# Optimization experiments

Measured on AMD Instinct MI355X. Metric: run time of the kernel, lower is better.

## Reference

```python
import jax, jax.numpy as jnp
import numpy as np

B, S, HID = 2, 4096, 768
H, DH = 12, 64
FF = 3072
W = 128  # one-sided attention band; window span = 2*W+1
EPS = 1e-12


def _ln(x, g, b):
    m = jnp.mean(x, axis=-1, keepdims=True)
    v = jnp.var(x, axis=-1, keepdims=True)
    return (x - m) * jax.lax.rsqrt(v + EPS) * g + b


def _band_attend(q, k, v, dmask, w):
    # q,k,v: (B,H,S,D) fp32; dmask: (B,S,2w+1) additive key-mask. Returns (B,S,H,D).
    b, h, s, d = q.shape
    nc = s // w
    qc = q.reshape(b, h, nc, w, d)
    pad = ((0, 0), (0, 0), (w, w), (0, 0))
    kp = jnp.pad(k, pad)
    vp = jnp.pad(v, pad)
    win = jnp.arange(nc)[:, None] * w + jnp.arange(3 * w)[None, :]  # (nc, 3w) indices into padded seq
    kc = kp[:, :, win]  # (B,H,nc,3w,D)
    vc = vp[:, :, win]
    s3 = jnp.einsum('bhcxd,bhcyd->bhcxy', qc, kc)  # (B,H,nc,w,3w)
    # extract band: query i in chunk attends keys j in [i, i+2w] of the 3w window
    off = jnp.arange(w)[:, None] + jnp.arange(2 * w + 1)[None, :]  # (w, 2w+1)
    band = jnp.take_along_axis(s3, off[None, None, None], axis=-1)  # (B,H,nc,w,2w+1)
    band = band.reshape(b, h, s, 2 * w + 1)
    keypos = jnp.arange(s)[:, None] + jnp.arange(-w, w + 1)[None, :]
    valid = (keypos >= 0) & (keypos < s)  # mask_invalid_locations
    band = jnp.where(valid[None, None], band, -1e30)
    band = band + dmask[:, None]
    p = jax.nn.softmax(band, axis=-1)
    # scatter probs back to chunk-dense (w, 3w) layout for the PV matmul
    pc = p.reshape(b, h, nc, w, 2 * w + 1)
    j = jnp.arange(3 * w)[None, :] - jnp.arange(w)[:, None]  # (w,3w) offset indices
    ok = (j >= 0) & (j <= 2 * w)
    jcl = jnp.clip(j, 0, 2 * w)
    pdense = jnp.take_along_axis(pc, jcl[None, None, None], axis=-1)  # (B,H,nc,w,3w)
    pdense = jnp.where(ok[None, None, None], pdense, 0.0)
    ctx = jnp.einsum('bhcxy,bhcyd->bhcxd', pdense, vc)  # (B,H,nc,w,D)
    return ctx.reshape(b, h, s, d).transpose(0, 2, 1, 3)


def setup_inputs() -> dict:
    key = jax.random.key(0)
    ks = jax.random.split(key, 8)
    sc = 0.02
    inp = {
        'hidden_states': jax.random.normal(ks[0], (B, S, HID), jnp.float32),
        'attention_mask': jax.random.randint(ks[1], (B, 1, 1, S), 0, 2, jnp.int32),
        'Wq': jax.random.normal(ks[2], (HID, HID), jnp.float32) * sc,
        'bq': jnp.zeros((HID,), jnp.float32),
        'Wk': jax.random.normal(ks[3], (HID, HID), jnp.float32) * sc,
        'bk': jnp.zeros((HID,), jnp.float32),
        'Wv': jax.random.normal(ks[4], (HID, HID), jnp.float32) * sc,
        'bv': jnp.zeros((HID,), jnp.float32),
        'Wd': jax.random.normal(ks[5], (HID, HID), jnp.float32) * sc,
        'bd': jnp.zeros((HID,), jnp.float32),
        'ln1_g': jnp.ones((HID,), jnp.float32),
        'ln1_b': jnp.zeros((HID,), jnp.float32),
        'Wf': jax.random.normal(ks[6], (HID, FF), jnp.float32) * sc,
        'bf': jnp.zeros((FF,), jnp.float32),
        'Wo': jax.random.normal(ks[7], (FF, HID), jnp.float32) * sc,
        'bo': jnp.zeros((HID,), jnp.float32),
        'ln2_g': jnp.ones((HID,), jnp.float32),
        'ln2_b': jnp.zeros((HID,), jnp.float32),
    }
    return inp


def reference(hidden_states, attention_mask, Wq, bq, Wk, bk, Wv, bv, Wd, bd,
              ln1_g, ln1_b, Wf, bf, Wo, bo, ln2_g, ln2_b):
    def heads(x):
        return x.reshape(B, S, H, DH).transpose(0, 2, 1, 3)  # (B,H,S,DH)

    q = heads(hidden_states @ Wq + bq).astype(jnp.float32) / np.float32(np.sqrt(DH))
    k = heads(hidden_states @ Wk + bk).astype(jnp.float32)
    v = heads(hidden_states @ Wv + bv).astype(jnp.float32)

    am = attention_mask.reshape(B, S)
    maskvals = jnp.where(am != 0, -10000.0, 0.0).astype(jnp.float32)  # (B,S)
    mpad = jnp.pad(maskvals, ((0, 0), (W, W)))
    kidx = jnp.arange(S)[:, None] + jnp.arange(2 * W + 1)[None, :]
    dmask = mpad[:, kidx]  # (B,S,2w+1)

    ctx = _band_attend(q, k, v, dmask, W)  # (B,S,H,DH)

    w_d = Wd.reshape(H, DH, HID)
    proj = jnp.einsum('bfnd,ndh->bfh', ctx, w_d) + bd
    attn_out = _ln(hidden_states + proj, ln1_g, ln1_b)

    ff = jax.nn.gelu(attn_out @ Wf + bf, approximate=False)
    ff = ff @ Wo + bo
    return _ln(ff + attn_out, ln2_g, ln2_b)
```

## Files before the change

### kernel.cpp

```cpp
#include <hip/hip_runtime.h>
#include <cstdint>
#include <cstddef>

#define S_LEN 4096
#define HIDD 768
#define NH 12
#define FFD 3072

typedef float f32x4 __attribute__((ext_vector_type(4)));
typedef short s16x8 __attribute__((ext_vector_type(8)));
typedef short s16x4 __attribute__((ext_vector_type(4)));

__device__ __forceinline__ short f2bf(float f) {
  unsigned u = __float_as_uint(f);
  u += 0x7fffu + ((u >> 16) & 1u);
  return (short)(u >> 16);
}
__device__ __forceinline__ float bf2f(short s) {
  return __uint_as_float(((unsigned)(unsigned short)s) << 16);
}

__global__ void convx_k(const float* __restrict__ x, short* __restrict__ o) {
  size_t i = (size_t)blockIdx.x * 256 + threadIdx.x;
  float4 f = ((const float4*)x)[i];
  s16x4 v;
  v[0] = f2bf(f.x); v[1] = f2bf(f.y); v[2] = f2bf(f.z); v[3] = f2bf(f.w);
  ((s16x4*)o)[i] = v;
}

__global__ void wtrans_k(const float* __restrict__ Wq, const float* __restrict__ Wk,
                         const float* __restrict__ Wv, const float* __restrict__ Wd,
                         const float* __restrict__ Wf, const float* __restrict__ Wo,
                         short* __restrict__ oq, short* __restrict__ ok_,
                         short* __restrict__ ov, short* __restrict__ od,
                         short* __restrict__ of_, short* __restrict__ oo) {
  __shared__ float tl[64][65];
  int id = blockIdx.x;
  const float* in; short* out; int R, C, tr, tc;
  if (id < 576) {
    int wsel = id / 144; int t = id % 144; tr = t / 12; tc = t % 12; R = 768; C = 768;
    in = wsel == 0 ? Wq : wsel == 1 ? Wk : wsel == 2 ? Wv : Wd;
    out = wsel == 0 ? oq : wsel == 1 ? ok_ : wsel == 2 ? ov : od;
  } else if (id < 1152) {
    int t = id - 576; tr = t / 48; tc = t % 48; R = 768; C = 3072; in = Wf; out = of_;
  } else {
    int t = id - 1152; tr = t / 12; tc = t % 12; R = 3072; C = 768; in = Wo; out = oo;
  }
  int r0 = tr * 64, c0 = tc * 64;
  int tid = threadIdx.x;
  #pragma unroll
  for (int i = 0; i < 16; i++) {
    int idx = i * 256 + tid; int r = idx >> 6, cc = idx & 63;
    tl[r][cc] = in[(size_t)(r0 + r) * C + c0 + cc];
  }
  __syncthreads();
  #pragma unroll
  for (int i = 0; i < 16; i++) {
    int idx = i * 256 + tid; int cc = idx >> 6, rr = idx & 63;
    out[(size_t)(c0 + cc) * R + r0 + rr] = f2bf(tl[rr][cc]);
  }
}

__global__ void vtrans_k(const short* __restrict__ vh, short* __restrict__ vth) {
  __shared__ short tl[64][72];
  int s0 = blockIdx.x * 64; int bh = blockIdx.y;
  int tid = threadIdx.x;
  const short* base = vh + ((size_t)bh << 18);
  #pragma unroll
  for (int i = 0; i < 16; i++) {
    int idx = i * 256 + tid; int r = idx >> 6, cc = idx & 63;
    tl[r][cc] = base[(size_t)(s0 + r) * 64 + cc];
  }
  __syncthreads();
  short* ob = vth + ((size_t)bh << 18);
  #pragma unroll
  for (int i = 0; i < 16; i++) {
    int idx = i * 256 + tid; int dh = idx >> 6, s = idx & 63;
    ob[((size_t)dh << 12) + s0 + s] = tl[s][dh];
  }
}

template <int EPI>
__global__ void __launch_bounds__(256) gemm_bt(
    const short* __restrict__ A, const short* __restrict__ Bt,
    const float* __restrict__ bias, const void* __restrict__ resid,
    void* __restrict__ out, int N, int K, float scale) {
  __shared__ short As[128 * 72];
  __shared__ short Bs[128 * 72];
  const int tid = threadIdx.x;
  const int lane = tid & 63;
  const int w = tid >> 6;
  const int wr = w >> 1, wc = w & 1;
  const int m0 = blockIdx.x * 128, n0 = blockIdx.y * 128;
  f32x4 acc[4][4];
  #pragma unroll
  for (int i = 0; i < 4; i++)
    #pragma unroll
    for (int j = 0; j < 4; j++) { acc[i][j][0] = 0.f; acc[i][j][1] = 0.f; acc[i][j][2] = 0.f; acc[i][j][3] = 0.f; }

  for (int k0 = 0; k0 < K; k0 += 64) {
    #pragma unroll
    for (int i = 0; i < 4; i++) {
      int ch = tid + i * 256;
      int row = ch >> 3, seg = ch & 7;
      *(s16x8*)&As[row * 72 + seg * 8] = *(const s16x8*)&A[(size_t)(m0 + row) * K + k0 + seg * 8];
      *(s16x8*)&Bs[row * 72 + seg * 8] = *(const s16x8*)&Bt[(size_t)(n0 + row) * K + k0 + seg * 8];
    }
    __syncthreads();
    const int kc = (lane >> 4) * 8;
    #pragma unroll
    for (int ks = 0; ks < 2; ks++) {
      s16x8 af[4], bfr[4];
      #pragma unroll
      for (int mt = 0; mt < 4; mt++)
        af[mt] = *(const s16x8*)&As[(wr * 64 + mt * 16 + (lane & 15)) * 72 + ks * 32 + kc];
      #pragma unroll
      for (int nt = 0; nt < 4; nt++)
        bfr[nt] = *(const s16x8*)&Bs[(wc * 64 + nt * 16 + (lane & 15)) * 72 + ks * 32 + kc];
      #pragma unroll
      for (int mt = 0; mt < 4; mt++)
        #pragma unroll
        for (int nt = 0; nt < 4; nt++)
          acc[mt][nt] = __builtin_amdgcn_mfma_f32_16x16x32_bf16(af[mt], bfr[nt], acc[mt][nt], 0, 0, 0);
    }
    __syncthreads();
  }
  #pragma unroll
  for (int nt = 0; nt < 4; nt++) {
    const int col = n0 + wc * 64 + nt * 16 + (lane & 15);
    const float bv = bias[col];
    #pragma unroll
    for (int mt = 0; mt < 4; mt++) {
      #pragma unroll
      for (int r = 0; r < 4; r++) {
        const int row = m0 + wr * 64 + mt * 16 + (lane >> 4) * 4 + r;
        float v = acc[mt][nt][r] + bv;
        if (EPI == 0) {
          int b = row >> 12, s = row & 4095, hh = col >> 6, dh = col & 63;
          ((short*)out)[((((size_t)b * NH + hh) * S_LEN + s) << 6) + dh] = f2bf(v * scale);
        } else if (EPI == 1) {
          float g = 0.5f * v * (1.f + erff(v * 0.70710678118f));
          ((short*)out)[(size_t)row * N + col] = f2bf(g);
        } else if (EPI == 2) {
          ((float*)out)[(size_t)row * N + col] = v + ((const float*)resid)[(size_t)row * N + col];
        } else {
          ((float*)out)[(size_t)row * N + col] = v + bf2f(((const short*)resid)[(size_t)row * N + col]);
        }
      }
    }
  }
}

__global__ void __launch_bounds__(512, 1) attn_k(
    const short* __restrict__ qh, const short* __restrict__ kh,
    const short* __restrict__ vth, const int* __restrict__ am,
    short* __restrict__ ctx) {
  extern __shared__ char smraw[];
  short* Kb = (short*)smraw;
  float* dmw = (float*)(smraw + 55296);
  short* Pb = (short*)(smraw + 56832);
  const int c = blockIdx.x;
  const int bh = blockIdx.y;
  const int b = bh / NH, hh = bh % NH;
  const int tid = threadIdx.x, lane = tid & 63, w = tid >> 6;
  const int q0 = c * 128, kw0 = q0 - 128;

  for (int ch = tid; ch < 3072; ch += 512) {
    int n = ch >> 3, seg = ch & 7;
    int kp = kw0 + n; kp = kp < 0 ? 0 : (kp > S_LEN - 1 ? S_LEN - 1 : kp);
    *(s16x8*)&Kb[n * 72 + seg * 8] = *(const s16x8*)&kh[(((size_t)bh * S_LEN + kp) << 6) + seg * 8];
  }
  for (int n = tid; n < 384; n += 512) {
    int kp = kw0 + n;
    float d;
    if (kp < 0 || kp >= S_LEN) d = -1e30f;
    else d = (am[b * S_LEN + kp] != 0) ? -10000.f : 0.f;
    dmw[n] = d;
  }
  __syncthreads();

  const short* qrow = qh + ((((size_t)bh * S_LEN) + q0 + w * 16 + (lane & 15)) << 6);
  s16x8 aq0 = *(const s16x8*)&qrow[(lane >> 4) * 8];
  s16x8 aq1 = *(const s16x8*)&qrow[32 + (lane >> 4) * 8];

  f32x4 sacc[24];
  #pragma unroll
  for (int t = 0; t < 24; t++) { sacc[t][0] = 0.f; sacc[t][1] = 0.f; sacc[t][2] = 0.f; sacc[t][3] = 0.f; }
  #pragma unroll
  for (int t = 0; t < 24; t++) {
    const short* kr = &Kb[(t * 16 + (lane & 15)) * 72 + (lane >> 4) * 8];
    s16x8 bk0 = *(const s16x8*)&kr[0];
    s16x8 bk1 = *(const s16x8*)&kr[32];
    sacc[t] = __builtin_amdgcn_mfma_f32_16x16x32_bf16(aq0, bk0, sacc[t], 0, 0, 0);
    sacc[t] = __builtin_amdgcn_mfma_f32_16x16x32_bf16(aq1, bk1, sacc[t], 0, 0, 0);
  }
  const int mbase = w * 16 + (lane >> 4) * 4;
  #pragma unroll
  for (int t = 0; t < 24; t++) {
    int n = t * 16 + (lane & 15);
    float d = dmw[n];
    #pragma unroll
    for (int r = 0; r < 4; r++) {
      int j = n - (mbase + r);
      float sv = sacc[t][r] + d;
      if (j < 0 || j > 256) sv = -1e30f;
      sacc[t][r] = sv;
    }
  }
  short* Pw = Pb + w * 16 * 392;
  #pragma unroll
  for (int r = 0; r < 4; r++) {
    float mx = -3e38f;
    #pragma unroll
    for (int t = 0; t < 24; t++) mx = fmaxf(mx, sacc[t][r]);
    #pragma unroll
    for (int d = 1; d < 16; d <<= 1) mx = fmaxf(mx, __shfl_xor(mx, d));
    float sum = 0.f;
    #pragma unroll
    for (int t = 0; t < 24; t++) { float p = __expf(sacc[t][r] - mx); sacc[t][r] = p; sum += p; }
    #pragma unroll
    for (int d = 1; d < 16; d <<= 1) sum += __shfl_xor(sum, d);
    float inv = 1.f / sum;
    #pragma unroll
    for (int t = 0; t < 24; t++)
      Pw[((lane >> 4) * 4 + r) * 392 + t * 16 + (lane & 15)] = f2bf(sacc[t][r] * inv);
  }
  __syncthreads();

  short* Vt = (short*)smraw;
  for (int ch = tid; ch < 3072; ch += 512) {
    int dh = ch / 48, seg = ch % 48;
    int n0 = seg * 8, kp0 = kw0 + n0;
    const short* vr = vth + (((size_t)bh * 64 + dh) << 12);
    s16x8 vv;
    if (kp0 >= 0 && kp0 + 7 < S_LEN) {
      vv = *(const s16x8*)&vr[kp0];
    } else {
      #pragma unroll
      for (int e = 0; e < 8; e++) {
        int kp = kp0 + e; kp = kp < 0 ? 0 : (kp > S_LEN - 1 ? S_LEN - 1 : kp);
        vv[e] = vr[kp];
      }
    }
    *(s16x8*)&Vt[dh * 392 + n0] = vv;
  }
  __syncthreads();

  f32x4 oacc[4];
  #pragma unroll
  for (int i = 0; i < 4; i++) { oacc[i][0] = 0.f; oacc[i][1] = 0.f; oacc[i][2] = 0.f; oacc[i][3] = 0.f; }
  #pragma unroll
  for (int ksp = 0; ksp < 12; ksp++) {
    s16x8 pa = *(const s16x8*)&Pw[(lane & 15) * 392 + ksp * 32 + (lane >> 4) * 8];
    #pragma unroll
    for (int ct = 0; ct < 4; ct++) {
      s16x8 vb = *(const s16x8*)&Vt[(ct * 16 + (lane & 15)) * 392 + ksp * 32 + (lane >> 4) * 8];
      oacc[ct] = __builtin_amdgcn_mfma_f32_16x16x32_bf16(pa, vb, oacc[ct], 0, 0, 0);
    }
  }
  #pragma unroll
  for (int ct = 0; ct < 4; ct++) {
    #pragma unroll
    for (int r = 0; r < 4; r++) {
      int srow = q0 + w * 16 + (lane >> 4) * 4 + r;
      int col = hh * 64 + ct * 16 + (lane & 15);
      ctx[((size_t)b * S_LEN + srow) * HIDD + col] = f2bf(oacc[ct][r]);
    }
  }
}

template <int OUTBF>
__global__ void ln_k(const float* __restrict__ in, const float* __restrict__ g,
                     const float* __restrict__ bb, void* __restrict__ out) {
  int row = blockIdx.x * 4 + (threadIdx.x >> 6);
  int lane = threadIdx.x & 63;
  const float4* x = (const float4*)(in + (size_t)row * HIDD);
  float4 v0 = x[lane], v1 = x[lane + 64], v2 = x[lane + 128];
  float s = v0.x + v0.y + v0.z + v0.w + v1.x + v1.y + v1.z + v1.w + v2.x + v2.y + v2.z + v2.w;
  float ss = v0.x * v0.x + v0.y * v0.y + v0.z * v0.z + v0.w * v0.w
           + v1.x * v1.x + v1.y * v1.y + v1.z * v1.z + v1.w * v1.w
           + v2.x * v2.x + v2.y * v2.y + v2.z * v2.z + v2.w * v2.w;
  #pragma unroll
  for (int d = 1; d < 64; d <<= 1) { s += __shfl_xor(s, d); ss += __shfl_xor(ss, d); }
  float mean = s * (1.f / 768.f);
  float var = ss * (1.f / 768.f) - mean * mean;
  float rs = rsqrtf(var + 1e-12f);
  const float4* gp = (const float4*)g;
  const float4* bp = (const float4*)bb;
  #pragma unroll
  for (int seg = 0; seg < 3; seg++) {
    int idx = lane + seg * 64;
    float4 vv = seg == 0 ? v0 : seg == 1 ? v1 : v2;
    float4 gg = gp[idx], b4 = bp[idx];
    float o0 = (vv.x - mean) * rs * gg.x + b4.x;
    float o1 = (vv.y - mean) * rs * gg.y + b4.y;
    float o2 = (vv.z - mean) * rs * gg.z + b4.z;
    float o3 = (vv.w - mean) * rs * gg.w + b4.w;
    if (OUTBF) {
      s16x4 o; o[0] = f2bf(o0); o[1] = f2bf(o1); o[2] = f2bf(o2); o[3] = f2bf(o3);
      ((s16x4*)out)[(size_t)row * 192 + idx] = o;
    } else {
      float4 o; o.x = o0; o.y = o1; o.z = o2; o.w = o3;
      ((float4*)out)[(size_t)row * 192 + idx] = o;
    }
  }
}

extern "C" void kernel_launch(void* const* d_in, const int* in_sizes, int n_in,
                              void* d_out, int out_size, void* d_ws, size_t ws_size,
                              hipStream_t stream) {
  const float* hid = (const float*)d_in[0];
  const int* am = (const int*)d_in[1];
  const float* Wq = (const float*)d_in[2];  const float* bq = (const float*)d_in[3];
  const float* Wk = (const float*)d_in[4];  const float* bk = (const float*)d_in[5];
  const float* Wv = (const float*)d_in[6];  const float* bv = (const float*)d_in[7];
  const float* Wd = (const float*)d_in[8];  const float* bd = (const float*)d_in[9];
  const float* g1 = (const float*)d_in[10]; const float* b1 = (const float*)d_in[11];
  const float* Wf = (const float*)d_in[12]; const float* bf = (const float*)d_in[13];
  const float* Wo = (const float*)d_in[14]; const float* bo = (const float*)d_in[15];
  const float* g2 = (const float*)d_in[16]; const float* b2 = (const float*)d_in[17];

  char* ws = (char*)d_ws;
  size_t off = 0;
  auto alloc = [&](size_t bytes) { char* p = ws + off; off += (bytes + 255) & ~(size_t)255; return p; };
  short* Xb   = (short*)alloc((size_t)8192 * 768 * 2);
  short* Wqb  = (short*)alloc((size_t)768 * 768 * 2);
  short* Wkb  = (short*)alloc((size_t)768 * 768 * 2);
  short* Wvb  = (short*)alloc((size_t)768 * 768 * 2);
  short* Wdb  = (short*)alloc((size_t)768 * 768 * 2);
  short* Wfb  = (short*)alloc((size_t)3072 * 768 * 2);
  short* Wob  = (short*)alloc((size_t)768 * 3072 * 2);
  short* qh   = (short*)alloc((size_t)8192 * 768 * 2);
  short* kh   = (short*)alloc((size_t)8192 * 768 * 2);
  short* vh   = (short*)alloc((size_t)8192 * 768 * 2);
  short* vth  = (short*)alloc((size_t)8192 * 768 * 2);
  short* ctx  = (short*)alloc((size_t)8192 * 768 * 2);
  short* aob  = (short*)alloc((size_t)8192 * 768 * 2);
  short* ffb  = (short*)alloc((size_t)8192 * 3072 * 2);
  float* f2r  = (float*)alloc((size_t)8192 * 768 * 4);
  float* ln1in = (float*)d_out;

  hipFuncSetAttribute(reinterpret_cast<const void*>(attn_k),
                      hipFuncAttributeMaxDynamicSharedMemorySize, 157184);

  convx_k<<<6144, 256, 0, stream>>>(hid, Xb);
  wtrans_k<<<1728, 256, 0, stream>>>(Wq, Wk, Wv, Wd, Wf, Wo, Wqb, Wkb, Wvb, Wdb, Wfb, Wob);

  dim3 g768(64, 6), g3072(64, 24);
  gemm_bt<0><<<g768, 256, 0, stream>>>(Xb, Wqb, bq, nullptr, qh, 768, 768, 0.125f);
  gemm_bt<0><<<g768, 256, 0, stream>>>(Xb, Wkb, bk, nullptr, kh, 768, 768, 1.f);
  gemm_bt<0><<<g768, 256, 0, stream>>>(Xb, Wvb, bv, nullptr, vh, 768, 768, 1.f);
  vtrans_k<<<dim3(64, 24), 256, 0, stream>>>(vh, vth);
  attn_k<<<dim3(32, 24), 512, 157184, stream>>>(qh, kh, vth, am, ctx);
  gemm_bt<2><<<g768, 256, 0, stream>>>(ctx, Wdb, bd, hid, ln1in, 768, 768, 1.f);
  ln_k<1><<<2048, 256, 0, stream>>>(ln1in, g1, b1, aob);
  gemm_bt<1><<<g3072, 256, 0, stream>>>(aob, Wfb, bf, nullptr, ffb, 3072, 768, 1.f);
  gemm_bt<3><<<g768, 256, 0, stream>>>(ffb, Wob, bo, aob, f2r, 768, 3072, 1.f);
  ln_k<0><<<2048, 256, 0, stream>>>(f2r, g2, b2, d_out);
}
```

Baseline: 302.0 us.

## Load GEMM tiles directly into LDS and fuse Q/K/V projections into one launch

The GEMM tile loads now use global_load_lds, which writes 16-byte chunks straight from global memory into shared memory without going through registers. To match that instruction's contiguous per-wave write pattern, the padded LDS row stride is dropped. The three Q, K and V projection GEMMs become a single launch over a 2304-wide output. The epilogue picks the bias, the scale and the output buffer per column, relying on the weight and output buffers being contiguous in the workspace. The cost is possible LDS bank conflicts on the MFMA fragment reads, since rows are no longer padded.

```diff
diff --git a/kernel.cpp b/kernel.cpp
--- a/kernel.cpp
+++ b/kernel.cpp
@@ -18,6 +18,12 @@
 }
 __device__ __forceinline__ float bf2f(short s) {
   return __uint_as_float(((unsigned)(unsigned short)s) << 16);
+}
+
+__device__ __forceinline__ void gload16(const short* g, short* l) {
+  __builtin_amdgcn_global_load_lds(
+      (__attribute__((address_space(1))) void*)(void*)const_cast<short*>(g),
+      (__attribute__((address_space(3))) void*)l, 16, 0, 0);
 }
 
 __global__ void convx_k(const float* __restrict__ x, short* __restrict__ o) {
@@ -83,28 +89,31 @@
 template <int EPI>
 __global__ void __launch_bounds__(256) gemm_bt(
     const short* __restrict__ A, const short* __restrict__ Bt,
-    const float* __restrict__ bias, const void* __restrict__ resid,
-    void* __restrict__ out, int N, int K, float scale) {
-  __shared__ short As[128 * 72];
-  __shared__ short Bs[128 * 72];
+    const float* __restrict__ bias, const float* __restrict__ bias1,
+    const float* __restrict__ bias2, const void* __restrict__ resid,
+    void* __restrict__ out, int N, int K) {
+  __shared__ __align__(16) short As[128 * 64];
+  __shared__ __align__(16) short Bs[128 * 64];
   const int tid = threadIdx.x;
   const int lane = tid & 63;
   const int w = tid >> 6;
   const int wr = w >> 1, wc = w & 1;
   const int m0 = blockIdx.x * 128, n0 = blockIdx.y * 128;
+  const int lr = lane >> 3, seg = lane & 7;
   f32x4 acc[4][4];
   #pragma unroll
   for (int i = 0; i < 4; i++)
     #pragma unroll
     for (int j = 0; j < 4; j++) { acc[i][j][0] = 0.f; acc[i][j][1] = 0.f; acc[i][j][2] = 0.f; acc[i][j][3] = 0.f; }
 
+  const short* Ab = A + (size_t)(m0 + lr) * K + seg * 8;
+  const short* Bb = Bt + (size_t)(n0 + lr) * K + seg * 8;
   for (int k0 = 0; k0 < K; k0 += 64) {
     #pragma unroll
     for (int i = 0; i < 4; i++) {
-      int ch = tid + i * 256;
-      int row = ch >> 3, seg = ch & 7;
-      *(s16x8*)&As[row * 72 + seg * 8] = *(const s16x8*)&A[(size_t)(m0 + row) * K + k0 + seg * 8];
-      *(s16x8*)&Bs[row * 72 + seg * 8] = *(const s16x8*)&Bt[(size_t)(n0 + row) * K + k0 + seg * 8];
+      const int ca = w * 4 + i;
+      gload16(Ab + (size_t)(ca * 8) * K + k0, &As[ca * 512]);
+      gload16(Bb + (size_t)(ca * 8) * K + k0, &Bs[ca * 512]);
     }
     __syncthreads();
     const int kc = (lane >> 4) * 8;
@@ -113,10 +122,10 @@
       s16x8 af[4], bfr[4];
       #pragma unroll
       for (int mt = 0; mt < 4; mt++)
-        af[mt] = *(const s16x8*)&As[(wr * 64 + mt * 16 + (lane & 15)) * 72 + ks * 32 + kc];
+        af[mt] = *(const s16x8*)&As[(wr * 64 + mt * 16 + (lane & 15)) * 64 + ks * 32 + kc];
       #pragma unroll
       for (int nt = 0; nt < 4; nt++)
-        bfr[nt] = *(const s16x8*)&Bs[(wc * 64 + nt * 16 + (lane & 15)) * 72 + ks * 32 + kc];
+        bfr[nt] = *(const s16x8*)&Bs[(wc * 64 + nt * 16 + (lane & 15)) * 64 + ks * 32 + kc];
       #pragma unroll
       for (int mt = 0; mt < 4; mt++)
         #pragma unroll
@@ -128,23 +137,39 @@
   #pragma unroll
   for (int nt = 0; nt < 4; nt++) {
     const int col = n0 + wc * 64 + nt * 16 + (lane & 15);
-    const float bv = bias[col];
-    #pragma unroll
-    for (int mt = 0; mt < 4; mt++) {
-      #pragma unroll
-      for (int r = 0; r < 4; r++) {
-        const int row = m0 + wr * 64 + mt * 16 + (lane >> 4) * 4 + r;
-        float v = acc[mt][nt][r] + bv;
-        if (EPI == 0) {
-          int b = row >> 12, s = row & 4095, hh = col >> 6, dh = col & 63;
-          ((short*)out)[((((size_t)b * NH + hh) * S_LEN + s) << 6) + dh] = f2bf(v * scale);
-        } else if (EPI == 1) {
-          float g = 0.5f * v * (1.f + erff(v * 0.70710678118f));
-          ((short*)out)[(size_t)row * N + col] = f2bf(g);
-        } else if (EPI == 2) {
-          ((float*)out)[(size_t)row * N + col] = v + ((const float*)resid)[(size_t)row * N + col];
-        } else {
-          ((float*)out)[(size_t)row * N + col] = v + bf2f(((const short*)resid)[(size_t)row * N + col]);
+    if (EPI == 0) {
+      const int cwhich = col >= 1536 ? 2 : (col >= 768 ? 1 : 0);
+      const int cwi = col - cwhich * 768;
+      const float* bsel = cwhich == 0 ? bias : (cwhich == 1 ? bias1 : bias2);
+      const float bvv = bsel[cwi];
+      const float sc = (cwhich == 0) ? 0.125f : 1.f;
+      const int hh = cwi >> 6, dh = cwi & 63;
+      short* outp = (short*)out + (size_t)cwhich * ((size_t)8192 * 768);
+      #pragma unroll
+      for (int mt = 0; mt < 4; mt++) {
+        #pragma unroll
+        for (int r = 0; r < 4; r++) {
+          const int row = m0 + wr * 64 + mt * 16 + (lane >> 4) * 4 + r;
+          const int b = row >> 12, s = row & 4095;
+          outp[((((size_t)b * NH + hh) * S_LEN + s) << 6) + dh] = f2bf((acc[mt][nt][r] + bvv) * sc);
+        }
+      }
+    } else {
+      const float bvv = bias[col];
+      #pragma unroll
+      for (int mt = 0; mt < 4; mt++) {
+        #pragma unroll
+        for (int r = 0; r < 4; r++) {
+          const int row = m0 + wr * 64 + mt * 16 + (lane >> 4) * 4 + r;
+          float v = acc[mt][nt][r] + bvv;
+          if (EPI == 1) {
+            float g = 0.5f * v * (1.f + erff(v * 0.70710678118f));
+            ((short*)out)[(size_t)row * N + col] = f2bf(g);
+          } else if (EPI == 2) {
+            ((float*)out)[(size_t)row * N + col] = v + ((const float*)resid)[(size_t)row * N + col];
+          } else {
+            ((float*)out)[(size_t)row * N + col] = v + bf2f(((const short*)resid)[(size_t)row * N + col]);
+          }
         }
       }
     }
@@ -339,6 +364,7 @@
   short* ffb  = (short*)alloc((size_t)8192 * 3072 * 2);
   float* f2r  = (float*)alloc((size_t)8192 * 768 * 4);
   float* ln1in = (float*)d_out;
+  (void)vh; (void)kh;
 
   hipFuncSetAttribute(reinterpret_cast<const void*>(attn_k),
                       hipFuncAttributeMaxDynamicSharedMemorySize, 157184);
@@ -346,15 +372,12 @@
   convx_k<<<6144, 256, 0, stream>>>(hid, Xb);
   wtrans_k<<<1728, 256, 0, stream>>>(Wq, Wk, Wv, Wd, Wf, Wo, Wqb, Wkb, Wvb, Wdb, Wfb, Wob);
 
-  dim3 g768(64, 6), g3072(64, 24);
-  gemm_bt<0><<<g768, 256, 0, stream>>>(Xb, Wqb, bq, nullptr, qh, 768, 768, 0.125f);
-  gemm_bt<0><<<g768, 256, 0, stream>>>(Xb, Wkb, bk, nullptr, kh, 768, 768, 1.f);
-  gemm_bt<0><<<g768, 256, 0, stream>>>(Xb, Wvb, bv, nullptr, vh, 768, 768, 1.f);
+  gemm_bt<0><<<dim3(64, 18), 256, 0, stream>>>(Xb, Wqb, bq, bk, bv, nullptr, qh, 2304, 768);
   vtrans_k<<<dim3(64, 24), 256, 0, stream>>>(vh, vth);
   attn_k<<<dim3(32, 24), 512, 157184, stream>>>(qh, kh, vth, am, ctx);
-  gemm_bt<2><<<g768, 256, 0, stream>>>(ctx, Wdb, bd, hid, ln1in, 768, 768, 1.f);
+  gemm_bt<2><<<dim3(64, 6), 256, 0, stream>>>(ctx, Wdb, bd, nullptr, nullptr, hid, ln1in, 768, 768);
   ln_k<1><<<2048, 256, 0, stream>>>(ln1in, g1, b1, aob);
-  gemm_bt<1><<<g3072, 256, 0, stream>>>(aob, Wfb, bf, nullptr, ffb, 3072, 768, 1.f);
-  gemm_bt<3><<<g768, 256, 0, stream>>>(ffb, Wob, bo, aob, f2r, 768, 3072, 1.f);
+  gemm_bt<1><<<dim3(64, 24), 256, 0, stream>>>(aob, Wfb, bf, nullptr, nullptr, nullptr, ffb, 3072, 768);
+  gemm_bt<3><<<dim3(64, 6), 256, 0, stream>>>(ffb, Wob, bo, nullptr, nullptr, aob, f2r, 768, 3072);
   ln_k<0><<<2048, 256, 0, stream>>>(f2r, g2, b2, d_out);
 }
```

After: 320.5 us. 1.06x slower.
